# Kernel optimization log

Measured on AMD Instinct MI355X. Metric: run time of the kernel, lower is better.

## Reference

```python
import jax, jax.numpy as jnp
import numpy as np

N, S, H, FA = 16, 64, 256, 256  # batch, sentences, memory_size, fact_attn_hidden


def setup_inputs() -> dict:
    key = jax.random.key(0)
    ks = jax.random.split(key, 12)
    g = lambda k, shp: (jax.random.normal(k, shp, jnp.float32) * 0.05)
    return dict(
        facts=jax.random.normal(ks[0], (N, S, H), jnp.float32),
        prevM=jax.random.normal(ks[1], (N, S, H), jnp.float32),
        questions=jax.random.normal(ks[2], (N, S, H), jnp.float32),
        doc_len=jax.random.randint(ks[3], (N,), S // 2, S + 1),
        z1_w=g(ks[4], (FA, 4 * H)), z1_b=jnp.zeros((FA,), jnp.float32),
        z2_w=g(ks[5], (1, FA)), z2_b=jnp.zeros((1,), jnp.float32),
        Wr_w=g(ks[6], (H, H)), Wr_b=jnp.zeros((H,), jnp.float32),
        Ur_w=g(ks[7], (H, H)), Ur_b=jnp.zeros((H,), jnp.float32),
        W_w=g(ks[8], (H, H)), W_b=jnp.zeros((H,), jnp.float32),
        U_w=g(ks[9], (H, H)), U_b=jnp.zeros((H,), jnp.float32),
        nm_w=g(ks[10], (H, 3 * H)), nm_b=jnp.zeros((H,), jnp.float32),
    )


def reference(facts, prevM, questions, doc_len,
              z1_w, z1_b, z2_w, z2_b,
              Wr_w, Wr_b, Ur_w, Ur_b, W_w, W_b, U_w, U_b,
              nm_w, nm_b):
    n, s, h = facts.shape
    # ---- make_interaction: pairwise features (query axis = dim1, fact/key axis = dim2)
    f = facts[:, None, :, :]       # (N,1,S,H) broadcast over queries
    m = prevM[:, :, None, :]       # (N,S,1,H) broadcast over keys
    q = questions[:, :, None, :]   # (N,S,1,H)
    z = jnp.concatenate([f * q, f * m, jnp.abs(f - q), jnp.abs(f - m)], axis=-1)  # (N,S,S,4H)
    Gh = jnp.tanh(z @ z1_w.T + z1_b)               # (N,S,S,FA)
    G = (Gh @ z2_w.T + z2_b)[..., 0]               # (N,S,S)
    mask = (jnp.arange(s) < doc_len[:, None]).astype(G.dtype)  # (N,S) key mask
    Gm = G * mask[:, None, :]
    Gm = jnp.where(Gm == 0, -jnp.inf, Gm)          # faithful to G[G==0] = -inf
    attn = jax.nn.softmax(Gm, axis=2)              # (N,S,S)

    # ---- AttentionalGRU over the S facts for each of the N*S query rows
    B = n * s
    fb = jnp.broadcast_to(facts[:, None], (n, s, s, h)).reshape(B, s, h)  # (B,S,H)
    gb = attn.reshape(B, s)                                               # (B,S)

    def step(C, xs):
        fact, gt = xs                                   # fact: (B,H), gt: (B,)
        r = jax.nn.sigmoid(fact @ Wr_w.T + Wr_b + C @ Ur_w.T + Ur_b)
        h_t = jnp.tanh(fact @ W_w.T + W_b + r * (C @ U_w.T + U_b))
        gt = gt[:, None]
        return gt * h_t + (1.0 - gt) * C, None

    C0 = jnp.zeros((B, h), facts.dtype)
    C, _ = jax.lax.scan(step, C0, (fb.transpose(1, 0, 2), gb.T))  # scan over S steps
    C = C.reshape(n, s, h)

    # ---- memory update (dropouts are identity in eval mode)
    concat = jnp.concatenate([prevM, C, questions], axis=-1)  # (N,S,3H)
    next_mem = jax.nn.relu(concat @ nm_w.T + nm_b)            # (N,S,H)
    return next_mem, attn
```

## Files before the change

### kernel.cpp

```cpp
#include <hip/hip_runtime.h>
#include <hip/hip_bf16.h>
#include <math.h>

#define NB 16
#define SS 64
#define HH 256
#define FAA 256

using short8 = __attribute__((ext_vector_type(8))) short;
using f32x4  = __attribute__((ext_vector_type(4))) float;

__device__ __forceinline__ unsigned int cvtpk(float a, float b) {
  unsigned int r;
  asm("v_cvt_pk_bf16_f32 %0, %1, %2" : "=v"(r) : "v"(a), "v"(b));
  return r;
}
__device__ __forceinline__ float sel4(const f32x4 a, int q) {
  const float s01 = (q & 1) ? a[1] : a[0];
  const float s23 = (q & 1) ? a[3] : a[2];
  return (q & 2) ? s23 : s01;
}

__global__ __launch_bounds__(256) void prolog_fused(
    const float* __restrict__ z1w, const float* __restrict__ Ur,
    const float* __restrict__ U, const float* __restrict__ nmw,
    const float* __restrict__ pm, const float* __restrict__ qs,
    unsigned short* __restrict__ z1wbf, unsigned short* __restrict__ wcatbf,
    unsigned short* __restrict__ nmbf, unsigned short* __restrict__ pmbf,
    unsigned short* __restrict__ qbf,
    const float* __restrict__ facts, const float* __restrict__ Wr,
    const float* __restrict__ Wrb, const float* __restrict__ Urb,
    const float* __restrict__ Ww, const float* __restrict__ Wb,
    float* __restrict__ FWr, float* __restrict__ FW) {
  __shared__ float fl[4][HH];
  const int bid = blockIdx.x, tid = threadIdx.x;

  auto cvt8 = [&](const float* src, unsigned short* dst, int base) {
    const float4 a = *(const float4*)(src + base);
    const float4 b = *(const float4*)(src + base + 4);
    uint4 o;
    o.x = cvtpk(a.x, a.y); o.y = cvtpk(a.z, a.w);
    o.z = cvtpk(b.x, b.y); o.w = cvtpk(b.z, b.w);
    *(uint4*)(dst + base) = o;
  };
  auto cvt8perm = [&](const float* row, unsigned short* dst, int sbase, int c0) {
    const float4 lo = *(const float4*)(row + c0);
    const float4 hi = *(const float4*)(row + c0 + 16);
    uint4 o;
    o.x = cvtpk(lo.x, hi.x); o.y = cvtpk(lo.y, hi.y);
    o.z = cvtpk(lo.z, hi.z); o.w = cvtpk(lo.w, hi.w);
    *(uint4*)(dst + sbase) = o;
  };

  if (bid < 128) {
    const int base = (bid * 256 + tid) * 8;
    cvt8(z1w, z1wbf, base);
    return;
  }
  if (bid < 192) {
    const int base = ((bid - 128) * 256 + tid) * 8;
    const int o = base >> 8, s0 = base & 255;
    const int gb = s0 & ~31, t0 = s0 & 31;
    const float* row = (o < 256) ? (Ur + o * 256) : (U + (o - 256) * 256);
    cvt8perm(row, wcatbf, base, gb + (t0 >> 1));
    return;
  }
  if (bid < 288) {
    const int base = ((bid - 192) * 256 + tid) * 8;
    const int o = base / 768, k0 = base - o * 768;
    const float* row = nmw + o * 768;
    if (k0 >= 256 && k0 < 512) {
      const int s0 = k0 - 256, gb = s0 & ~31, t0 = s0 & 31;
      cvt8perm(row, nmbf, base, 256 + gb + (t0 >> 1));
    } else {
      cvt8(row, nmbf + o * 768, k0);
    }
    return;
  }
  if (bid < 416) {
    const int base = ((bid - 288) * 256 + tid) * 8;
    cvt8(pm, pmbf, base);
    return;
  }
  if (bid < 544) {
    const int base = ((bid - 416) * 256 + tid) * 8;
    cvt8(qs, qbf, base);
    return;
  }
  const int b0 = (bid - 544) * 4;
#pragma unroll
  for (int r = 0; r < 4; ++r) fl[r][tid] = facts[(b0 + r) * HH + tid];
  __syncthreads();
  float ar[4] = {0.f, 0.f, 0.f, 0.f}, aw[4] = {0.f, 0.f, 0.f, 0.f};
  const float4* wr = (const float4*)(Wr + tid * HH);
  const float4* ww = (const float4*)(Ww + tid * HH);
  for (int d4 = 0; d4 < 64; ++d4) {
    float4 a = wr[d4], b = ww[d4];
#pragma unroll
    for (int r = 0; r < 4; ++r) {
      float4 f = *(const float4*)&fl[r][d4 * 4];
      ar[r] += a.x * f.x + a.y * f.y + a.z * f.z + a.w * f.w;
      aw[r] += b.x * f.x + b.y * f.y + b.z * f.z + b.w * f.w;
    }
  }
  const float br = Wrb[tid] + Urb[tid], bw = Wb[tid];
#pragma unroll
  for (int r = 0; r < 4; ++r) {
    FWr[(b0 + r) * HH + tid] = ar[r] + br;
    FW[(b0 + r) * HH + tid] = aw[r] + bw;
  }
}

__global__ __launch_bounds__(512, 4) void gate_gemm(
    const float* __restrict__ facts, const float* __restrict__ prevM,
    const float* __restrict__ questions, const unsigned short* __restrict__ z1wbf,
    const float* __restrict__ z1b, const float* __restrict__ z2w,
    const float* __restrict__ z2b, const int* __restrict__ doc_len,
    float* __restrict__ attn) {
  __shared__ unsigned short Ab[2][128 * 32];
  __shared__ unsigned short Bb[2][256 * 32];
  __shared__ float Gpart[128][4];

  const int bi = blockIdx.x;
  const int n = bi >> 5, i0 = (bi & 31) * 2;
  const int tid = threadIdx.x;
  const int w = tid >> 6, l = tid & 63;
  const int rg = w >> 2, cg = w & 3;
  const int l15 = l & 15, q = l >> 4;
  const int t15 = tid & 15, jb = tid >> 4;

  const float* fn = facts + n * SS * HH;
  const float* qn = questions + (n * SS + i0) * HH;
  const float* mn = prevM + (n * SS + i0) * HH;

  auto stageB = [&](int buf, int hc, int s) {
    const int kb = s * 256 + hc * 32;
    const int swz = ((l & 3) ^ ((l >> 2) & 3)) * 8;
#pragma unroll
    for (int j = 0; j < 2; ++j) {
      const int colg = w * 32 + j * 16 + (l >> 2);
      const unsigned short* src = z1wbf + colg * 1024 + kb + swz;
      __builtin_amdgcn_global_load_lds(src, Bb[buf] + (w * 32 + j * 16) * 32, 16, 0, 0);
    }
  };

  auto buildA = [&](int buf, int s, float2 f0, float2 f1, float2 q0, float2 q1,
                    float2 m0, float2 m1) {
    unsigned int* dst = (unsigned int*)Ab[buf];
    const int dsw = t15 ^ ((jb & 3) << 2);
    const float2 o0 = (s & 1) ? m0 : q0;
    const float2 o1 = (s & 1) ? m1 : q1;
#pragma unroll
    for (int pl = 0; pl < 2; ++pl) {
      const float fx = pl ? f1.x : f0.x;
      const float fy = pl ? f1.y : f0.y;
#pragma unroll
      for (int il = 0; il < 2; ++il) {
        const int row = il * 64 + pl * 32 + jb;
        const float ox = il ? o1.x : o0.x;
        const float oy = il ? o1.y : o0.y;
        float a, b;
        if (s < 2) { a = fx * ox;         b = fy * oy; }
        else       { a = fabsf(fx - ox);  b = fabsf(fy - oy); }
        dst[row * 16 + dsw] = cvtpk(a, b);
      }
    }
  };

  const f32x4 zero4 = {0.f, 0.f, 0.f, 0.f};
  f32x4 acc[4][4];
#pragma unroll
  for (int a = 0; a < 4; ++a)
#pragma unroll
    for (int b = 0; b < 4; ++b) acc[a][b] = zero4;

  auto mfmaStep = [&](int buf) {
    short8 Bfr[4];
#pragma unroll
    for (int nf = 0; nf < 4; ++nf) {
      const int col = cg * 64 + nf * 16 + l15;
      Bfr[nf] = *(const short8*)&Bb[buf][col * 32 + (q ^ (l15 & 3)) * 8];
    }
    __builtin_amdgcn_s_setprio(1);
#pragma unroll
    for (int mf = 0; mf < 4; ++mf) {
      const int row = rg * 64 + mf * 16 + l15;
      const short8 Afm = *(const short8*)&Ab[buf][row * 32 + (q ^ (l15 & 3)) * 8];
#pragma unroll
      for (int nf = 0; nf < 4; ++nf)
        acc[mf][nf] = __builtin_amdgcn_mfma_f32_16x16x32_bf16(Afm, Bfr[nf], acc[mf][nf], 0, 0, 0);
    }
    __builtin_amdgcn_s_setprio(0);
  };

  const int hh2 = t15 * 2;
  auto pf = [&](int hc, float2& f0, float2& f1, float2& q0, float2& q1,
                float2& m0, float2& m1) {
    const int h = hc * 32 + hh2;
    f0 = *(const float2*)(fn + jb * HH + h);
    f1 = *(const float2*)(fn + (jb + 32) * HH + h);
    q0 = *(const float2*)(qn + h);
    q1 = *(const float2*)(qn + HH + h);
    m0 = *(const float2*)(mn + h);
    m1 = *(const float2*)(mn + HH + h);
  };

  float2 Rf0, Rf1, Rq0, Rq1, Rm0, Rm1;
  float2 Sf0, Sf1, Sq0, Sq1, Sm0, Sm1;
  pf(0, Rf0, Rf1, Rq0, Rq1, Rm0, Rm1);
  stageB(0, 0, 0);
  buildA(0, 0, Rf0, Rf1, Rq0, Rq1, Rm0, Rm1);
  __syncthreads();

  int buf = 0;
  for (int hc = 0; hc < 8; ++hc) {
    stageB(buf ^ 1, hc, 1);
    buildA(buf ^ 1, 1, Rf0, Rf1, Rq0, Rq1, Rm0, Rm1);
    mfmaStep(buf);
    __syncthreads();
    buf ^= 1;
    stageB(buf ^ 1, hc, 2);
    buildA(buf ^ 1, 2, Rf0, Rf1, Rq0, Rq1, Rm0, Rm1);
    mfmaStep(buf);
    __syncthreads();
    buf ^= 1;
    stageB(buf ^ 1, hc, 3);
    buildA(buf ^ 1, 3, Rf0, Rf1, Rq0, Rq1, Rm0, Rm1);
    if (hc < 7) pf(hc + 1, Sf0, Sf1, Sq0, Sq1, Sm0, Sm1);
    mfmaStep(buf);
    __syncthreads();
    buf ^= 1;
    if (hc < 7) {
      stageB(buf ^ 1, hc + 1, 0);
      buildA(buf ^ 1, 0, Sf0, Sf1, Sq0, Sq1, Sm0, Sm1);
    }
    mfmaStep(buf);
    __syncthreads();
    buf ^= 1;
    Rf0 = Sf0; Rf1 = Sf1; Rq0 = Sq0; Rq1 = Sq1; Rm0 = Sm0; Rm1 = Sm1;
  }

  float psum[4][4];
#pragma unroll
  for (int mf = 0; mf < 4; ++mf)
#pragma unroll
    for (int v = 0; v < 4; ++v) psum[mf][v] = 0.f;

#pragma unroll
  for (int nf = 0; nf < 4; ++nf) {
    const int k = cg * 64 + nf * 16 + l15;
    const float zb = z1b[k], zw = z2w[k];
#pragma unroll
    for (int mf = 0; mf < 4; ++mf)
#pragma unroll
      for (int v = 0; v < 4; ++v) {
        const float x = acc[mf][nf][v] + zb;
        const float e = __expf(2.f * x);
        const float t = 1.f - 2.f / (e + 1.f);
        psum[mf][v] += zw * t;
      }
  }
#pragma unroll
  for (int d = 1; d < 16; d <<= 1)
#pragma unroll
    for (int mf = 0; mf < 4; ++mf)
#pragma unroll
      for (int v = 0; v < 4; ++v) psum[mf][v] += __shfl_xor(psum[mf][v], d, 64);
  if (l15 == 0) {
#pragma unroll
    for (int mf = 0; mf < 4; ++mf)
#pragma unroll
      for (int v = 0; v < 4; ++v)
        Gpart[rg * 64 + mf * 16 + q * 4 + v][cg] = psum[mf][v];
  }
  __syncthreads();
  if (tid < 128) {
    const float gg = Gpart[tid][0] + Gpart[tid][1] + Gpart[tid][2] + Gpart[tid][3] + z2b[0];
    const int i = i0 + (tid >> 6), j = tid & 63;
    const int dl = doc_len[n];
    const float x = (j < dl && gg != 0.0f) ? gg : -INFINITY;
    float mx = x;
#pragma unroll
    for (int d = 1; d < 64; d <<= 1) mx = fmaxf(mx, __shfl_xor(mx, d, 64));
    const float e = (x == -INFINITY) ? 0.f : __expf(x - mx);
    float s = e;
#pragma unroll
    for (int d = 1; d < 64; d <<= 1) s += __shfl_xor(s, d, 64);
    attn[(n * SS + i) * SS + j] = e / s;
  }
}

__global__ __launch_bounds__(512, 2) void gru_scan(
    const unsigned short* __restrict__ wcat, const float* __restrict__ FWr,
    const float* __restrict__ FW, const float* __restrict__ Ub,
    const float* __restrict__ attn, unsigned short* __restrict__ Cout) {
  __shared__ unsigned short Cbf[2][4 * 272];
  __shared__ float attn_sT[64 * 4];

  const int bi = blockIdx.x, n = bi >> 4, i0 = (bi & 15) * 4;
  const int tid = threadIdx.x, w = tid >> 6, l = tid & 63;
  const int l15 = l & 15, q = l >> 4;
  const int h0 = w * 32 + l15;

  short8 Bf[8][4];
#pragma unroll
  for (int f = 0; f < 4; ++f) {
    const int wrow = ((f >> 1) ? 256 : 0) + w * 32 + (f & 1) * 16 + l15;
    const unsigned short* bb = wcat + wrow * 256 + q * 8;
#pragma unroll
    for (int kt = 0; kt < 8; ++kt)
      Bf[kt][f] = *(const short8*)(bb + kt * 32);
  }

  const float ub0 = Ub[h0], ub1 = Ub[h0 + 16];

  for (int e = tid; e < 64 * 4; e += 512)
    attn_sT[e] = attn[(n * SS + i0 + (e & 3)) * SS + (e >> 2)];
  for (int e = tid; e < 544; e += 512)
    ((unsigned int*)Cbf[0])[e] = 0u;
  __syncthreads();

  const float* fwr_g = FWr + n * SS * HH;
  const float* fw_g  = FW + n * SS * HH;

  float cm0 = 0.f, cm1 = 0.f;
  float fr0 = fwr_g[h0], fr1 = fwr_g[h0 + 16];
  float fc0 = fw_g[h0],  fc1 = fw_g[h0 + 16];

  for (int t = 0; t < 64; ++t) {
    const int cur = t & 1;
    const unsigned short* Cr = Cbf[cur];
    unsigned int* Cw = (unsigned int*)Cbf[cur ^ 1];

    short8 Af[8];
    const int arow = (l15 & 3) * 272;
#pragma unroll
    for (int kt = 0; kt < 8; ++kt)
      Af[kt] = *(const short8*)&Cr[arow + kt * 32 + q * 8];

    float nr0 = 0.f, nr1 = 0.f, nc0 = 0.f, nc1 = 0.f;
    if (t < 63) {
      nr0 = fwr_g[(t + 1) * HH + h0];
      nr1 = fwr_g[(t + 1) * HH + h0 + 16];
      nc0 = fw_g[(t + 1) * HH + h0];
      nc1 = fw_g[(t + 1) * HH + h0 + 16];
    }

    const f32x4 z4 = {0.f, 0.f, 0.f, 0.f};
    f32x4 a0 = z4, a1 = z4, a2 = z4, a3 = z4;
    __builtin_amdgcn_s_setprio(1);
#pragma unroll
    for (int kt = 0; kt < 8; ++kt) {
      a0 = __builtin_amdgcn_mfma_f32_16x16x32_bf16(Af[kt], Bf[kt][0], a0, 0, 0, 0);
      a2 = __builtin_amdgcn_mfma_f32_16x16x32_bf16(Af[kt], Bf[kt][2], a2, 0, 0, 0);
    }
#pragma unroll
    for (int kt = 0; kt < 8; ++kt) {
      a1 = __builtin_amdgcn_mfma_f32_16x16x32_bf16(Af[kt], Bf[kt][1], a1, 0, 0, 0);
      a3 = __builtin_amdgcn_mfma_f32_16x16x32_bf16(Af[kt], Bf[kt][3], a3, 0, 0, 0);
    }
    __builtin_amdgcn_s_setprio(0);

    const float g = attn_sT[t * 4 + q];

    const float yr0 = sel4(a0, q), yu0 = sel4(a2, q);
    const float r0 = 1.f / (1.f + __expf(-(fr0 + yr0)));
    const float x0 = fc0 + r0 * (yu0 + ub0);
    const float e0 = __expf(2.f * x0);
    const float h0t = 1.f - 2.f / (e0 + 1.f);
    cm0 += g * (h0t - cm0);

    const float yr1 = sel4(a1, q), yu1 = sel4(a3, q);
    const float r1 = 1.f / (1.f + __expf(-(fr1 + yr1)));
    const float x1 = fc1 + r1 * (yu1 + ub1);
    const float e1 = __expf(2.f * x1);
    const float h1t = 1.f - 2.f / (e1 + 1.f);
    cm1 += g * (h1t - cm1);

    Cw[q * 136 + w * 16 + l15] = cvtpk(cm0, cm1);

    fr0 = nr0; fr1 = nr1; fc0 = nc0; fc1 = nc1;
    __syncthreads();
  }

  {
    const int row = tid >> 7, wo = tid & 127;
    ((unsigned int*)Cout)[(n * SS + i0 + row) * 128 + wo] =
        *(const unsigned int*)&Cbf[0][row * 272 + wo * 2];
  }
}

__global__ __launch_bounds__(256) void next_mem_gemm(
    const unsigned short* __restrict__ pmbf, const unsigned short* __restrict__ cbf,
    const unsigned short* __restrict__ qbf, const unsigned short* __restrict__ nmbf,
    const float* __restrict__ nmb, float* __restrict__ out) {
  __shared__ unsigned short A[64][40];
  const int bi = blockIdx.x;
  const int rb = bi >> 3, cb = bi & 7;
  const int r0 = rb * 64, c0 = cb * 32;
  const int tid = threadIdx.x, w = tid >> 6, l = tid & 63;
  const int l15 = l & 15, q = l >> 4;

  f32x4 acc[2];
  const f32x4 z4 = {0.f, 0.f, 0.f, 0.f};
#pragma unroll
  for (int nf = 0; nf < 2; ++nf) acc[nf] = z4;

  for (int kt = 0; kt < 24; ++kt) {
    const int kg = kt * 32;
    const unsigned short* src =
        kg < 256 ? (pmbf + kg) : (kg < 512 ? (cbf + kg - 256) : (qbf + kg - 512));
    const int kk = (tid & 15) * 2;
#pragma unroll
    for (int ps = 0; ps < 4; ++ps) {
      const int row = ps * 16 + (tid >> 4);
      *(unsigned int*)&A[row][kk] = *(const unsigned int*)(src + (r0 + row) * HH + kk);
    }
    __syncthreads();
    short8 Bfr[2];
#pragma unroll
    for (int nf = 0; nf < 2; ++nf)
      Bfr[nf] = *(const short8*)(nmbf + (c0 + nf * 16 + l15) * 768 + kg + q * 8);
    const short8 Af = *(const short8*)&A[w * 16 + l15][q * 8];
#pragma unroll
    for (int nf = 0; nf < 2; ++nf)
      acc[nf] = __builtin_amdgcn_mfma_f32_16x16x32_bf16(Af, Bfr[nf], acc[nf], 0, 0, 0);
    __syncthreads();
  }
#pragma unroll
  for (int nf = 0; nf < 2; ++nf) {
    const int col = c0 + nf * 16 + l15;
    const float bv = nmb[col];
#pragma unroll
    for (int v = 0; v < 4; ++v) {
      const int grow = r0 + w * 16 + q * 4 + v;
      out[grow * HH + col] = fmaxf(acc[nf][v] + bv, 0.f);
    }
  }
}

extern "C" void kernel_launch(void* const* d_in, const int* in_sizes, int n_in,
                              void* d_out, int out_size, void* d_ws, size_t ws_size,
                              hipStream_t stream) {
  const float* facts     = (const float*)d_in[0];
  const float* prevM     = (const float*)d_in[1];
  const float* questions = (const float*)d_in[2];
  const int*   doc_len   = (const int*)d_in[3];
  const float* z1w = (const float*)d_in[4];
  const float* z1b = (const float*)d_in[5];
  const float* z2w = (const float*)d_in[6];
  const float* z2b = (const float*)d_in[7];
  const float* Wrw = (const float*)d_in[8];
  const float* Wrb = (const float*)d_in[9];
  const float* Urw = (const float*)d_in[10];
  const float* Urb = (const float*)d_in[11];
  const float* Ww  = (const float*)d_in[12];
  const float* Wb  = (const float*)d_in[13];
  const float* Uw  = (const float*)d_in[14];
  const float* Ub  = (const float*)d_in[15];
  const float* nmw = (const float*)d_in[16];
  const float* nmb = (const float*)d_in[17];

  char* ws = (char*)d_ws;
  unsigned short* z1wbf  = (unsigned short*)(ws + 0);
  unsigned short* wcatbf = (unsigned short*)(ws + 524288);
  unsigned short* nmbf   = (unsigned short*)(ws + 786432);
  unsigned short* pmbf   = (unsigned short*)(ws + 1179648);
  unsigned short* qbf    = (unsigned short*)(ws + 1703936);
  float* FWr = (float*)(ws + 2490368);
  float* FW  = (float*)(ws + 3538944);
  unsigned short* cbf = (unsigned short*)(ws + 4587520);

  float* out  = (float*)d_out;
  float* attn = out + NB * SS * HH;

  prolog_fused<<<800, 256, 0, stream>>>(z1w, Urw, Uw, nmw, prevM, questions,
                                        z1wbf, wcatbf, nmbf, pmbf, qbf,
                                        facts, Wrw, Wrb, Urb, Ww, Wb, FWr, FW);
  gate_gemm<<<512, 512, 0, stream>>>(facts, prevM, questions, z1wbf, z1b, z2w, z2b,
                                     doc_len, attn);
  gru_scan<<<256, 512, 0, stream>>>(wcatbf, FWr, FW, Ub, attn, cbf);
  next_mem_gemm<<<128, 256, 0, stream>>>(pmbf, cbf, qbf, nmbf, nmb, out);
}
```

Before: 246.3 us.

## Triple-buffer gate GEMM LDS staging with partial vmcnt waits

```diff
diff --git a/kernel.cpp b/kernel.cpp
--- a/kernel.cpp
+++ b/kernel.cpp
@@ -117,8 +117,8 @@
     const float* __restrict__ z1b, const float* __restrict__ z2w,
     const float* __restrict__ z2b, const int* __restrict__ doc_len,
     float* __restrict__ attn) {
-  __shared__ unsigned short Ab[2][128 * 32];
-  __shared__ unsigned short Bb[2][256 * 32];
+  __shared__ unsigned short Ab[3][128 * 32];
+  __shared__ unsigned short Bb[3][256 * 32];
   __shared__ float Gpart[128][4];
 
   const int bi = blockIdx.x;
@@ -133,8 +133,8 @@
   const float* qn = questions + (n * SS + i0) * HH;
   const float* mn = prevM + (n * SS + i0) * HH;
 
-  auto stageB = [&](int buf, int hc, int s) {
-    const int kb = s * 256 + hc * 32;
+  auto stageB = [&](int buf, int c) {
+    const int kb = (c & 3) * 256 + (c >> 2) * 32;
     const int swz = ((l & 3) ^ ((l >> 2) & 3)) * 8;
 #pragma unroll
     for (int j = 0; j < 2; ++j) {
@@ -208,36 +208,38 @@
   float2 Rf0, Rf1, Rq0, Rq1, Rm0, Rm1;
   float2 Sf0, Sf1, Sq0, Sq1, Sm0, Sm1;
   pf(0, Rf0, Rf1, Rq0, Rq1, Rm0, Rm1);
-  stageB(0, 0, 0);
+  stageB(0, 0);
+  stageB(1, 1);
   buildA(0, 0, Rf0, Rf1, Rq0, Rq1, Rm0, Rm1);
-  __syncthreads();
-
-  int buf = 0;
-  for (int hc = 0; hc < 8; ++hc) {
-    stageB(buf ^ 1, hc, 1);
-    buildA(buf ^ 1, 1, Rf0, Rf1, Rq0, Rq1, Rm0, Rm1);
-    mfmaStep(buf);
-    __syncthreads();
-    buf ^= 1;
-    stageB(buf ^ 1, hc, 2);
-    buildA(buf ^ 1, 2, Rf0, Rf1, Rq0, Rq1, Rm0, Rm1);
-    mfmaStep(buf);
-    __syncthreads();
-    buf ^= 1;
-    stageB(buf ^ 1, hc, 3);
-    buildA(buf ^ 1, 3, Rf0, Rf1, Rq0, Rq1, Rm0, Rm1);
-    if (hc < 7) pf(hc + 1, Sf0, Sf1, Sq0, Sq1, Sm0, Sm1);
-    mfmaStep(buf);
-    __syncthreads();
-    buf ^= 1;
-    if (hc < 7) {
-      stageB(buf ^ 1, hc + 1, 0);
-      buildA(buf ^ 1, 0, Sf0, Sf1, Sq0, Sq1, Sm0, Sm1);
-    }
-    mfmaStep(buf);
-    __syncthreads();
-    buf ^= 1;
-    Rf0 = Sf0; Rf1 = Sf1; Rq0 = Sq0; Rq1 = Sq1; Rm0 = Sm0; Rm1 = Sm1;
+  asm volatile("s_waitcnt vmcnt(2) lgkmcnt(0)\n\ts_barrier" ::: "memory");
+
+#pragma unroll
+  for (int c = 0; c < 32; ++c) {
+    const int s = c & 3, hc = c >> 2;
+    const int cb = c % 3, nb2 = (c + 1) % 3, fb = (c + 2) % 3;
+    const bool pfphase = (s == 2) && (hc < 7);
+
+    if (c + 2 < 32) stageB(fb, c + 2);
+    if (pfphase) pf(hc + 1, Sf0, Sf1, Sq0, Sq1, Sm0, Sm1);
+    if (c + 1 < 32) {
+      if (((c + 1) & 3) == 0)
+        buildA(nb2, 0, Sf0, Sf1, Sq0, Sq1, Sm0, Sm1);
+      else
+        buildA(nb2, (c + 1) & 3, Rf0, Rf1, Rq0, Rq1, Rm0, Rm1);
+    }
+    mfmaStep(cb);
+
+    if (c <= 29) {
+      if (pfphase)
+        asm volatile("s_waitcnt vmcnt(8) lgkmcnt(0)\n\ts_barrier" ::: "memory");
+      else
+        asm volatile("s_waitcnt vmcnt(2) lgkmcnt(0)\n\ts_barrier" ::: "memory");
+    } else if (c == 30) {
+      asm volatile("s_waitcnt vmcnt(0) lgkmcnt(0)\n\ts_barrier" ::: "memory");
+    }
+    if (s == 3) {
+      Rf0 = Sf0; Rf1 = Sf1; Rq0 = Sq0; Rq1 = Sq1; Rm0 = Sm0; Rm1 = Sm1;
+    }
   }
 
   float psum[4][4];
```

After: 242.1 us. About the same (-1.7%).
